# Kernel tuning notes

Hardware: AMD Instinct MI355X
Metric: run time of the kernel (lower is better)

## Reference

```python
import jax, jax.numpy as jnp
import numpy as np
from functools import partial

N_OSC = 50
N_PER = 40
DT = 0.001
STEPS = 700
HALF_PI = float(np.pi / 2)
# limb constants (simple antagonist-muscle one-link limb, as in TorchOneLinkMuscleLimb)
R_MOM = 0.02      # muscle moment arm
L0 = 0.1          # muscle length at angle 0
INERTIA = 1e-3
DAMP = 0.01
K_MUS = 50.0
L_REST = 0.05
TAU_M = 0.05


def get_m1_length(theta):
    return L0 - R_MOM * theta


def get_m2_length(theta):
    return L0 + R_MOM * theta


def limb_f(l_state, activation):
    # l_state: (B,4) = (angle, ang. velocity, m1 length, m2 length); activation: (B,2)
    theta, omega, l1, l2 = l_state[:, 0], l_state[:, 1], l_state[:, 2], l_state[:, 3]
    f1 = jax.nn.relu(activation[:, 0]) * K_MUS * jax.nn.relu(l1 - L_REST)
    f2 = jax.nn.relu(activation[:, 1]) * K_MUS * jax.nn.relu(l2 - L_REST)
    domega = (R_MOM * (f2 - f1) - DAMP * omega) / INERTIA
    dl1 = (get_m1_length(theta) - l1) / TAU_M
    dl2 = (get_m2_length(theta) - l2) / TAU_M
    return jnp.stack([omega, domega, dl1, dl2], axis=1)


def setup_inputs() -> dict:
    key = jax.random.key(0)
    ks = jax.random.split(key, 16)
    B = 4096
    x = jax.random.normal(ks[0], (B, 2), dtype=jnp.float32) * 0.5
    def lin(k, out_d, in_d, scale=None):
        s = (1.0 / np.sqrt(in_d)) if scale is None else scale
        kw, kb = jax.random.split(k)
        w = jax.random.uniform(kw, (out_d, in_d), jnp.float32, -s, s)
        b = jax.random.uniform(kb, (out_d,), jnp.float32, -s, s)
        return w, b
    fc1_w, fc1_b = lin(ks[1], 128, 2)
    fc2_w, fc2_b = lin(ks[2], 128, 128)
    fc3_w, fc3_b = lin(ks[3], N_OSC * 2, 128)
    fcd_w, fcd_b = lin(ks[4], 2, 128)
    fcd_w = fcd_w / 100.0
    fcd_b = fcd_b * 0.0 + 0.1
    fc4_w, fc4_b = lin(ks[5], 32, N_OSC * N_PER)
    fc5_w, fc5_b = lin(ks[6], 2, 32)
    fc5_w = fc5_w / 10000.0
    fc5_b = fc5_b * 0.0
    # NEF oscillator populations: encoders (unit vectors), biases, decoders
    enc = jax.random.normal(ks[7], (N_OSC, N_PER, 2), dtype=jnp.float32)
    enc = enc / jnp.linalg.norm(enc, axis=-1, keepdims=True)
    osc_bias = jax.random.uniform(ks[8], (N_OSC, N_PER), jnp.float32, -1.0, 1.0)
    dec = jax.random.normal(ks[9], (N_OSC, 2, N_PER), dtype=jnp.float32) * 0.05
    return dict(x=x, fc1_w=fc1_w, fc1_b=fc1_b, fc2_w=fc2_w, fc2_b=fc2_b,
                fc3_w=fc3_w, fc3_b=fc3_b, fcd_w=fcd_w, fcd_b=fcd_b,
                enc=enc, osc_bias=osc_bias, dec=dec,
                fc4_w=fc4_w, fc4_b=fc4_b, fc5_w=fc5_w, fc5_b=fc5_b)


def _forward(x, fc1_w, fc1_b, fc2_w, fc2_b, fc3_w, fc3_b, fcd_w, fcd_b,
             enc, osc_bias, dec, fc4_w, fc4_b, fc5_w, fc5_b):
    B = x.shape[0]
    current_angle = x[:, 0]
    h = jax.nn.relu(x @ fc1_w.T + fc1_b)
    direct = h @ fcd_w.T + fcd_b                     # (B, 2)
    h2 = jax.nn.relu(h @ fc2_w.T + fc2_b)
    xo = h2 @ fc3_w.T + fc3_b                        # (B, 2*N_OSC)
    o0 = jnp.transpose(xo.reshape(B, N_OSC, 2), (1, 0, 2))   # (O, B, 2)
    l0 = jnp.stack([current_angle, jnp.zeros_like(current_angle),
                    get_m1_length(current_angle), get_m2_length(current_angle)], axis=1)

    def step(carry, _):
        o_states, l_state = carry
        # NEF activities: relu(encoders . state + bias) per oscillator
        a = jax.nn.relu(jnp.einsum('opd,obd->obp', enc, o_states) + osc_bias[:, None, :])  # (O,B,P)
        deriv = jnp.einsum('odp,obp->obd', dec, a)
        o_states = o_states + DT * deriv
        activities = jnp.transpose(a, (1, 0, 2)).reshape(B, N_OSC * N_PER)  # (B, 2000)
        b1 = jax.nn.relu(activities @ fc4_w.T + fc4_b)
        activation = b1 @ fc5_w.T + fc5_b + direct    # (B, 2)
        l_new = l_state + DT * limb_f(l_state, activation)
        pos, vel = l_new[:, 0], l_new[:, 1]
        in_bounds = (pos > -HALF_PI) & (pos < HALF_PI)
        l_new = jnp.stack([jnp.clip(pos, -HALF_PI, HALF_PI),
                           jnp.where(in_bounds, vel, 0.0),
                           l_new[:, 2], l_new[:, 3]], axis=1)
        return (o_states, l_new), (l_new, activation)

    (_, _), (l_states, activations) = jax.lax.scan(step, (o0, l0), None, length=STEPS)
    return l_states, activations


@jax.jit
def reference(x, fc1_w, fc1_b, fc2_w, fc2_b, fc3_w, fc3_b, fcd_w, fcd_b,
              enc, osc_bias, dec, fc4_w, fc4_b, fc5_w, fc5_b):
    return _forward(x, fc1_w, fc1_b, fc2_w, fc2_b, fc3_w, fc3_b, fcd_w, fcd_b,
                    enc, osc_bias, dec, fc4_w, fc4_b, fc5_w, fc5_b)
```

## Files before the change

### kernel.cpp

```cpp
#include <hip/hip_runtime.h>

#define NTHR 1024
#define NB   16
#define NOSC 50
#define NPER 40
#define KTOT 2000
#define KPAD 2048
#define NSTEP 700
#define BATCH 4096
#define B1STR 36
#define OS_STR 36
#define HALF_PI 1.57079632679489662f
#define ACT_OFF ((size_t)NSTEP * BATCH * 4)

typedef _Float16 v8h __attribute__((ext_vector_type(8)));
typedef _Float16 h2_t __attribute__((ext_vector_type(2)));
typedef float v4f __attribute__((ext_vector_type(4)));

__device__ _Float16 g_w4[32 * KPAD];

__device__ __forceinline__ float fdot2f(float a_bits, float b_bits, float acc) {
    h2_t a = __builtin_bit_cast(h2_t, a_bits);
    h2_t b = __builtin_bit_cast(h2_t, b_bits);
#if __has_builtin(__builtin_amdgcn_fdot2)
    return __builtin_amdgcn_fdot2(a, b, acc, false);
#else
    return fmaf((float)a[0], (float)b[0], fmaf((float)a[1], (float)b[1], acc));
#endif
}

__device__ __forceinline__ float dot4(float4 a, float4 b, float acc) {
    acc = fmaf(a.x, b.x, acc);
    acc = fmaf(a.y, b.y, acc);
    acc = fmaf(a.z, b.z, acc);
    acc = fmaf(a.w, b.w, acc);
    return acc;
}

__device__ __forceinline__ float pkrtz(float a, float b) {
    auto q = __builtin_amdgcn_cvt_pkrtz(a, b);
    return __builtin_bit_cast(float, q);
}

__device__ __forceinline__ float cvt2rtn(float a, float b) {
    h2_t u; u[0] = (_Float16)a; u[1] = (_Float16)b;
    return __builtin_bit_cast(float, u);
}

__global__ void prep_f16(const float* __restrict__ fc4_w) {
    int tid = blockIdx.x * blockDim.x + threadIdx.x;
    int j = tid >> 11, k = tid & 2047;
    g_w4[j * KPAD + k] = (k < KTOT) ? (_Float16)fc4_w[j * KTOT + k] : (_Float16)0.f;
}

__global__ __launch_bounds__(NTHR)
void net_main(const float* __restrict__ x,
              const float* __restrict__ fc1_w, const float* __restrict__ fc1_b,
              const float* __restrict__ fc2_w, const float* __restrict__ fc2_b,
              const float* __restrict__ fc3_w, const float* __restrict__ fc3_b,
              const float* __restrict__ fcd_w, const float* __restrict__ fcd_b,
              const float* __restrict__ enc,   const float* __restrict__ osc_bias,
              const float* __restrict__ dec,
              const float* __restrict__ fc4_b,
              const float* __restrict__ fc5_w, const float* __restrict__ fc5_b,
              float* __restrict__ out)
{
    __shared__ __align__(16) _Float16 act_sh[256 * 128];
    __shared__ __align__(16) float part[8 * 2 * 256];
    __shared__ __align__(16) float os_sh[NOSC * OS_STR];
    __shared__ __align__(16) float b1s[NB * B1STR];
    __shared__ __align__(16) float dir[NB * 2];

    const int t    = threadIdx.x;
    const int lane = t & 63;
    const int wv   = t >> 6;
    const int b0   = blockIdx.x * NB;

    float* h  = (float*)act_sh;
    float* h2 = (float*)act_sh + NB * 128;

    #pragma unroll
    for (int ii = 0; ii < 2; ++ii) {
        int task = t + ii * NTHR;
        int b = task >> 7, i = task & 127;
        float x0 = x[(b0 + b) * 2 + 0];
        float x1 = x[(b0 + b) * 2 + 1];
        float v = fmaf(x0, fc1_w[2 * i], fmaf(x1, fc1_w[2 * i + 1], fc1_b[i]));
        h[b * 128 + i] = fmaxf(v, 0.f);
    }
    __syncthreads();
    #pragma unroll
    for (int ii = 0; ii < 2; ++ii) {
        int task = t + ii * NTHR;
        int b = task >> 7, i = task & 127;
        float acc = fc2_b[i];
        #pragma unroll 4
        for (int k = 0; k < 128; k += 4)
            acc = dot4(*(const float4*)&fc2_w[i * 128 + k],
                       *(const float4*)&h[b * 128 + k], acc);
        h2[b * 128 + i] = fmaxf(acc, 0.f);
    }
    if (t < NB * 2) {
        int b = t >> 1, j = t & 1;
        float acc = fcd_b[j];
        #pragma unroll 4
        for (int k = 0; k < 128; k += 4)
            acc = dot4(*(const float4*)&fcd_w[j * 128 + k],
                       *(const float4*)&h[b * 128 + k], acc);
        dir[b * 2 + j] = acc;
    }
    __syncthreads();
    #pragma unroll
    for (int ii = 0; ii < 2; ++ii) {
        int task = t + ii * NTHR;
        if (task < NOSC * NB * 2) {
            int o = task >> 5, r = task & 31, b = r >> 1;
            int row = o * 2 + (r & 1);
            float acc = fc3_b[row];
            #pragma unroll 4
            for (int k = 0; k < 128; k += 4)
                acc = dot4(*(const float4*)&fc3_w[row * 128 + k],
                           *(const float4*)&h2[b * 128 + k], acc);
            os_sh[o * OS_STR + r] = acc;
        }
    }
    const int my_oct = t >> 2;
    float4 e0 = {0,0,0,0}, e1 = {0,0,0,0}, e2 = {0,0,0,0}, e3 = {0,0,0,0};
    float4 bi0 = {0,0,0,0}, bi1 = {0,0,0,0};
    int my_o = 0;
    if (my_oct < 250) {
        const float4* ep = (const float4*)&enc[my_oct * 16];
        e0 = ep[0]; e1 = ep[1]; e2 = ep[2]; e3 = ep[3];
        const float4* bp = (const float4*)&osc_bias[my_oct * 8];
        bi0 = bp[0]; bi1 = bp[1];
        my_o = my_oct / 5;
    }
    const int di = t - 512;
    int d_o = 0, d_b = 0;
    bool dual = false;
    if (di >= 0) {
        if (di < 288) { dual = true; d_o = di >> 3; d_b = (di & 7) * 2; }
        else          { int task = di + 288; d_o = task >> 4; d_b = task & 15; }
    }
    float theta = 0.f, omega = 0.f, l1 = 0.f, l2 = 0.f, bs0 = 0.f, bs1 = 0.f;
    const int cb = t - 1008;
    if (cb >= 0 && cb < NB) {
        theta = x[(b0 + cb) * 2 + 0];
        l1 = fmaf(-0.02f, theta, 0.1f);
        l2 = fmaf( 0.02f, theta, 0.1f);
    }
    __syncthreads();
    if (cb >= 0 && cb < NB) {
        bs0 = dir[cb * 2 + 0] + fc5_b[0];
        bs1 = dir[cb * 2 + 1] + fc5_b[1];
    }
    if (t < 768) act_sh[32000 + t] = (_Float16)0.f;

    const int n_col = lane & 15, quad = lane >> 4;
    const int lidx  = lane ^ (quad << 2);
    int a_off[8];
    #pragma unroll
    for (int ks = 0; ks < 8; ++ks) {
        int oct = wv * 32 + ks * 4 + quad;
        a_off[ks] = (oct & 255) * 128 + ((n_col ^ (oct & 15)) * 8);
    }

    v4f st[16];
    if (t < 512) {
        const _Float16* wp = &g_w4[n_col * KPAD + wv * 256 + quad * 8];
        #pragma unroll
        for (int ks = 0; ks < 8; ++ks) {
            st[ks]     = __builtin_bit_cast(v4f, *(const v8h*)&wp[ks * 32]);
            st[8 + ks] = __builtin_bit_cast(v4f, *(const v8h*)&wp[16 * KPAD + ks * 32]);
        }
    } else {
        const float* d0p = &dec[(d_o * 2 + 0) * 40];
        const float* d1p = &dec[(d_o * 2 + 1) * 40];
        #pragma unroll
        for (int c = 0; c < 5; ++c) {
            v4f v0, v1;
            v0.x = cvt2rtn(d0p[c*8+0], d0p[c*8+1]);
            v0.y = cvt2rtn(d0p[c*8+2], d0p[c*8+3]);
            v0.z = cvt2rtn(d0p[c*8+4], d0p[c*8+5]);
            v0.w = cvt2rtn(d0p[c*8+6], d0p[c*8+7]);
            v1.x = cvt2rtn(d1p[c*8+0], d1p[c*8+1]);
            v1.y = cvt2rtn(d1p[c*8+2], d1p[c*8+3]);
            v1.z = cvt2rtn(d1p[c*8+4], d1p[c*8+5]);
            v1.w = cvt2rtn(d1p[c*8+6], d1p[c*8+7]);
            st[c]     = v0;
            st[5 + c] = v1;
        }
        #pragma unroll
        for (int i = 10; i < 16; ++i) st[i] = (v4f){0.f, 0.f, 0.f, 0.f};
    }

    auto phaseA = [&]() {
        if (my_oct < 250) {
            const int i4 = (t & 3) << 2;
            float4 osA = *(const float4*)&os_sh[my_o * OS_STR + i4 * 2];
            float4 osB = *(const float4*)&os_sh[my_o * OS_STR + i4 * 2 + 4];
            #pragma unroll
            for (int ii = 0; ii < 4; ++ii) {
                int b = i4 + ii;
                float osx = (ii == 0) ? osA.x : (ii == 1) ? osA.z : (ii == 2) ? osB.x : osB.z;
                float osy = (ii == 0) ? osA.y : (ii == 1) ? osA.w : (ii == 2) ? osB.y : osB.w;
                float r0 = fmaxf(fmaf(e0.x, osx, fmaf(e0.y, osy, bi0.x)), 0.f);
                float r1 = fmaxf(fmaf(e0.z, osx, fmaf(e0.w, osy, bi0.y)), 0.f);
                float r2 = fmaxf(fmaf(e1.x, osx, fmaf(e1.y, osy, bi0.z)), 0.f);
                float r3 = fmaxf(fmaf(e1.z, osx, fmaf(e1.w, osy, bi0.w)), 0.f);
                float r4 = fmaxf(fmaf(e2.x, osx, fmaf(e2.y, osy, bi1.x)), 0.f);
                float r5 = fmaxf(fmaf(e2.z, osx, fmaf(e2.w, osy, bi1.y)), 0.f);
                float r6 = fmaxf(fmaf(e3.x, osx, fmaf(e3.y, osy, bi1.z)), 0.f);
                float r7 = fmaxf(fmaf(e3.z, osx, fmaf(e3.w, osy, bi1.w)), 0.f);
                float4 pk;
                pk.x = pkrtz(r0, r1);
                pk.y = pkrtz(r2, r3);
                pk.z = pkrtz(r4, r5);
                pk.w = pkrtz(r6, r7);
                *(float4*)&act_sh[my_oct * 128 + ((b ^ my_oct) & 15) * 8] = pk;
            }
        }
    };

    auto derivDot = [&](int b, float& pOut, float& qOut) {
        float p0 = 0.f, p1 = 0.f, q0 = 0.f, q1 = 0.f;
        #pragma unroll
        for (int c = 0; c < 5; ++c) {
            int oct = d_o * 5 + c;
            float4 af = *(const float4*)&act_sh[oct * 128 + ((b ^ oct) & 15) * 8];
            p0 = fdot2f(af.x, st[c].x, p0);     p1 = fdot2f(af.y, st[c].y, p1);
            p0 = fdot2f(af.z, st[c].z, p0);     p1 = fdot2f(af.w, st[c].w, p1);
            q0 = fdot2f(af.x, st[5+c].x, q0);   q1 = fdot2f(af.y, st[5+c].y, q1);
            q0 = fdot2f(af.z, st[5+c].z, q0);   q1 = fdot2f(af.w, st[5+c].w, q1);
        }
        pOut = p0 + p1;
        qOut = q0 + q1;
    };

    phaseA();
    __syncthreads();

    for (int s = 0; s < NSTEP; ++s) {
        if (t < 512) {
            v4f c0 = {0.f, 0.f, 0.f, 0.f}, c1 = {0.f, 0.f, 0.f, 0.f};
            #pragma unroll
            for (int ks = 0; ks < 8; ++ks) {
                v8h a  = *(const v8h*)&act_sh[a_off[ks]];
                v8h w0 = __builtin_bit_cast(v8h, st[ks]);
                v8h w1 = __builtin_bit_cast(v8h, st[8 + ks]);
                c0 = __builtin_amdgcn_mfma_f32_16x16x32_f16(a, w0, c0, 0, 0, 0);
                c1 = __builtin_amdgcn_mfma_f32_16x16x32_f16(a, w1, c1, 0, 0, 0);
            }
            *(v4f*)&part[(wv * 2 + 0) * 256 + lidx * 4] = c0;
            *(v4f*)&part[(wv * 2 + 1) * 256 + lidx * 4] = c1;
        } else {
            if (dual) {
                float pA, qA, pB, qB;
                derivDot(d_b,     pA, qA);
                derivDot(d_b + 1, pB, qB);
                float4 osv = *(const float4*)&os_sh[d_o * OS_STR + d_b * 2];
                osv.x += 0.001f * pA;
                osv.y += 0.001f * qA;
                osv.z += 0.001f * pB;
                osv.w += 0.001f * qB;
                *(float4*)&os_sh[d_o * OS_STR + d_b * 2] = osv;
            } else {
                float p, q;
                derivDot(d_b, p, q);
                float2 osv = *(const float2*)&os_sh[d_o * OS_STR + d_b * 2];
                osv.x += 0.001f * p;
                osv.y += 0.001f * q;
                *(float2*)&os_sh[d_o * OS_STR + d_b * 2] = osv;
            }
            if (cb >= 0 && cb < NB && s > 0) {
                float a0 = bs0, a1 = bs1;
                #pragma unroll
                for (int i = 0; i < 32; i += 4) {
                    float4 bv = *(const float4*)&b1s[cb * B1STR + i];
                    a0 = dot4(bv, *(const float4*)&fc5_w[i],      a0);
                    a1 = dot4(bv, *(const float4*)&fc5_w[32 + i], a1);
                }
                float f1v = fmaxf(a0, 0.f) * 50.f * fmaxf(l1 - 0.05f, 0.f);
                float f2v = fmaxf(a1, 0.f) * 50.f * fmaxf(l2 - 0.05f, 0.f);
                float domega = (0.02f * (f2v - f1v) - 0.01f * omega) / 0.001f;
                float dl1 = ((0.1f - 0.02f * theta) - l1) / 0.05f;
                float dl2 = ((0.1f + 0.02f * theta) - l2) / 0.05f;
                float pos = fmaf(0.001f, omega,  theta);
                float vel = fmaf(0.001f, domega, omega);
                l1 = fmaf(0.001f, dl1, l1);
                l2 = fmaf(0.001f, dl2, l2);
                bool inb = (pos > -HALF_PI) && (pos < HALF_PI);
                float posc = fminf(fmaxf(pos, -HALF_PI), HALF_PI);
                vel = inb ? vel : 0.f;
                theta = posc;
                omega = vel;
                float4 lo; lo.x = posc; lo.y = vel; lo.z = l1; lo.w = l2;
                *(float4*)&out[((size_t)(s - 1) * BATCH + (b0 + cb)) * 4] = lo;
                float2 ao; ao.x = a0; ao.y = a1;
                *(float2*)&out[ACT_OFF + ((size_t)(s - 1) * BATCH + (b0 + cb)) * 2] = ao;
            }
        }
        __syncthreads();

        if (t < 512) {
            int b = t & 15, j = t >> 4;
            int g = j >> 4, n = j & 15;
            int Lp = (b >> 2) * 16 + (n ^ ((b >> 2) << 2));
            int base = g * 256 + Lp * 4 + (b & 3);
            float sum = 0.f;
            #pragma unroll
            for (int w = 0; w < 8; ++w)
                sum += part[w * 512 + base];
            b1s[b * B1STR + j] = fmaxf(sum + fc4_b[j], 0.f);
        }
        phaseA();
        __syncthreads();
    }

    if (cb >= 0 && cb < NB) {
        const int s = NSTEP - 1;
        float a0 = bs0, a1 = bs1;
        #pragma unroll
        for (int i = 0; i < 32; i += 4) {
            float4 bv = *(const float4*)&b1s[cb * B1STR + i];
            a0 = dot4(bv, *(const float4*)&fc5_w[i],      a0);
            a1 = dot4(bv, *(const float4*)&fc5_w[32 + i], a1);
        }
        float f1v = fmaxf(a0, 0.f) * 50.f * fmaxf(l1 - 0.05f, 0.f);
        float f2v = fmaxf(a1, 0.f) * 50.f * fmaxf(l2 - 0.05f, 0.f);
        float domega = (0.02f * (f2v - f1v) - 0.01f * omega) / 0.001f;
        float dl1 = ((0.1f - 0.02f * theta) - l1) / 0.05f;
        float dl2 = ((0.1f + 0.02f * theta) - l2) / 0.05f;
        float pos = fmaf(0.001f, omega,  theta);
        float vel = fmaf(0.001f, domega, omega);
        l1 = fmaf(0.001f, dl1, l1);
        l2 = fmaf(0.001f, dl2, l2);
        bool inb = (pos > -HALF_PI) && (pos < HALF_PI);
        float posc = fminf(fmaxf(pos, -HALF_PI), HALF_PI);
        vel = inb ? vel : 0.f;
        float4 lo; lo.x = posc; lo.y = vel; lo.z = l1; lo.w = l2;
        *(float4*)&out[((size_t)s * BATCH + (b0 + cb)) * 4] = lo;
        float2 ao; ao.x = a0; ao.y = a1;
        *(float2*)&out[ACT_OFF + ((size_t)s * BATCH + (b0 + cb)) * 2] = ao;
    }
}

extern "C" void kernel_launch(void* const* d_in, const int* in_sizes, int n_in,
                              void* d_out, int out_size, void* d_ws, size_t ws_size,
                              hipStream_t stream) {
    (void)in_sizes; (void)n_in; (void)d_ws; (void)ws_size; (void)out_size;
    const float* x_     = (const float*)d_in[0];
    const float* fc1_w  = (const float*)d_in[1];
    const float* fc1_b  = (const float*)d_in[2];
    const float* fc2_w  = (const float*)d_in[3];
    const float* fc2_b  = (const float*)d_in[4];
    const float* fc3_w  = (const float*)d_in[5];
    const float* fc3_b  = (const float*)d_in[6];
    const float* fcd_w  = (const float*)d_in[7];
    const float* fcd_b  = (const float*)d_in[8];
    const float* enc    = (const float*)d_in[9];
    const float* oscb   = (const float*)d_in[10];
    const float* dec    = (const float*)d_in[11];
    const float* fc4_w  = (const float*)d_in[12];
    const float* fc4_b  = (const float*)d_in[13];
    const float* fc5_w  = (const float*)d_in[14];
    const float* fc5_b  = (const float*)d_in[15];
    float* out = (float*)d_out;

    hipLaunchKernelGGL(prep_f16, dim3(256), dim3(256), 0, stream, fc4_w);
    hipLaunchKernelGGL(net_main, dim3(BATCH / NB), dim3(NTHR), 0, stream,
                       x_, fc1_w, fc1_b, fc2_w, fc2_b, fc3_w, fc3_b,
                       fcd_w, fcd_b, enc, oscb, dec, fc4_b,
                       fc5_w, fc5_b, out);
}
```

Baseline: 1.995 ms.

## Double-buffer fc4 partials and skew b1 reduction and limb update by a step

Double-buffers the MFMA partial-sum buffer and the b1 activation buffer so the fc4 reduction for step s-1 runs in the MFMA waves during step s, and the fc5/limb update trails by two steps. This takes the b1 reduction out of the serial section between the two barriers, shortening the critical path per step. In exchange it uses more LDS, adds an epilogue to drain the pipeline, and lengthens the MFMA warps' critical work.

```diff
diff --git a/kernel.cpp b/kernel.cpp
--- a/kernel.cpp
+++ b/kernel.cpp
@@ -66,9 +66,9 @@
               float* __restrict__ out)
 {
     __shared__ __align__(16) _Float16 act_sh[256 * 128];
-    __shared__ __align__(16) float part[8 * 2 * 256];
+    __shared__ __align__(16) float part[2 * 4096];
     __shared__ __align__(16) float os_sh[NOSC * OS_STR];
-    __shared__ __align__(16) float b1s[NB * B1STR];
+    __shared__ __align__(16) float b1s[2][NB * B1STR];
     __shared__ __align__(16) float dir[NB * 2];
 
     const int t    = threadIdx.x;
@@ -237,11 +237,40 @@
         qOut = q0 + q1;
     };
 
+    auto fc5Limb = [&](int sm) {
+        float a0 = bs0, a1 = bs1;
+        #pragma unroll
+        for (int i = 0; i < 32; i += 4) {
+            float4 bv = *(const float4*)&b1s[sm & 1][cb * B1STR + i];
+            a0 = dot4(bv, *(const float4*)&fc5_w[i],      a0);
+            a1 = dot4(bv, *(const float4*)&fc5_w[32 + i], a1);
+        }
+        float f1v = fmaxf(a0, 0.f) * 50.f * fmaxf(l1 - 0.05f, 0.f);
+        float f2v = fmaxf(a1, 0.f) * 50.f * fmaxf(l2 - 0.05f, 0.f);
+        float domega = (0.02f * (f2v - f1v) - 0.01f * omega) / 0.001f;
+        float dl1 = ((0.1f - 0.02f * theta) - l1) / 0.05f;
+        float dl2 = ((0.1f + 0.02f * theta) - l2) / 0.05f;
+        float pos = fmaf(0.001f, omega,  theta);
+        float vel = fmaf(0.001f, domega, omega);
+        l1 = fmaf(0.001f, dl1, l1);
+        l2 = fmaf(0.001f, dl2, l2);
+        bool inb = (pos > -HALF_PI) && (pos < HALF_PI);
+        float posc = fminf(fmaxf(pos, -HALF_PI), HALF_PI);
+        vel = inb ? vel : 0.f;
+        theta = posc;
+        omega = vel;
+        float4 lo; lo.x = posc; lo.y = vel; lo.z = l1; lo.w = l2;
+        *(float4*)&out[((size_t)sm * BATCH + (b0 + cb)) * 4] = lo;
+        float2 ao; ao.x = a0; ao.y = a1;
+        *(float2*)&out[ACT_OFF + ((size_t)sm * BATCH + (b0 + cb)) * 2] = ao;
+    };
+
     phaseA();
     __syncthreads();
 
     for (int s = 0; s < NSTEP; ++s) {
         if (t < 512) {
+            const int pb = (s & 1) * 4096;
             v4f c0 = {0.f, 0.f, 0.f, 0.f}, c1 = {0.f, 0.f, 0.f, 0.f};
             #pragma unroll
             for (int ks = 0; ks < 8; ++ks) {
@@ -251,8 +280,20 @@
                 c0 = __builtin_amdgcn_mfma_f32_16x16x32_f16(a, w0, c0, 0, 0, 0);
                 c1 = __builtin_amdgcn_mfma_f32_16x16x32_f16(a, w1, c1, 0, 0, 0);
             }
-            *(v4f*)&part[(wv * 2 + 0) * 256 + lidx * 4] = c0;
-            *(v4f*)&part[(wv * 2 + 1) * 256 + lidx * 4] = c1;
+            *(v4f*)&part[pb + (wv * 2 + 0) * 256 + lidx * 4] = c0;
+            *(v4f*)&part[pb + (wv * 2 + 1) * 256 + lidx * 4] = c1;
+            if (s > 0) {
+                const int pr = ((s - 1) & 1) * 4096;
+                int b = t & 15, j = t >> 4;
+                int g = j >> 4, n = j & 15;
+                int Lp = (b >> 2) * 16 + (n ^ ((b >> 2) << 2));
+                int base = pr + g * 256 + Lp * 4 + (b & 3);
+                float sum = 0.f;
+                #pragma unroll
+                for (int w = 0; w < 8; ++w)
+                    sum += part[w * 512 + base];
+                b1s[(s - 1) & 1][b * B1STR + j] = fmaxf(sum + fc4_b[j], 0.f);
+            }
         } else {
             if (dual) {
                 float pA, qA, pB, qB;
@@ -272,77 +313,32 @@
                 osv.y += 0.001f * q;
                 *(float2*)&os_sh[d_o * OS_STR + d_b * 2] = osv;
             }
-            if (cb >= 0 && cb < NB && s > 0) {
-                float a0 = bs0, a1 = bs1;
-                #pragma unroll
-                for (int i = 0; i < 32; i += 4) {
-                    float4 bv = *(const float4*)&b1s[cb * B1STR + i];
-                    a0 = dot4(bv, *(const float4*)&fc5_w[i],      a0);
-                    a1 = dot4(bv, *(const float4*)&fc5_w[32 + i], a1);
-                }
-                float f1v = fmaxf(a0, 0.f) * 50.f * fmaxf(l1 - 0.05f, 0.f);
-                float f2v = fmaxf(a1, 0.f) * 50.f * fmaxf(l2 - 0.05f, 0.f);
-                float domega = (0.02f * (f2v - f1v) - 0.01f * omega) / 0.001f;
-                float dl1 = ((0.1f - 0.02f * theta) - l1) / 0.05f;
-                float dl2 = ((0.1f + 0.02f * theta) - l2) / 0.05f;
-                float pos = fmaf(0.001f, omega,  theta);
-                float vel = fmaf(0.001f, domega, omega);
-                l1 = fmaf(0.001f, dl1, l1);
-                l2 = fmaf(0.001f, dl2, l2);
-                bool inb = (pos > -HALF_PI) && (pos < HALF_PI);
-                float posc = fminf(fmaxf(pos, -HALF_PI), HALF_PI);
-                vel = inb ? vel : 0.f;
-                theta = posc;
-                omega = vel;
-                float4 lo; lo.x = posc; lo.y = vel; lo.z = l1; lo.w = l2;
-                *(float4*)&out[((size_t)(s - 1) * BATCH + (b0 + cb)) * 4] = lo;
-                float2 ao; ao.x = a0; ao.y = a1;
-                *(float2*)&out[ACT_OFF + ((size_t)(s - 1) * BATCH + (b0 + cb)) * 2] = ao;
-            }
+            if (cb >= 0 && cb < NB && s >= 2)
+                fc5Limb(s - 2);
         }
         __syncthreads();
 
-        if (t < 512) {
-            int b = t & 15, j = t >> 4;
-            int g = j >> 4, n = j & 15;
-            int Lp = (b >> 2) * 16 + (n ^ ((b >> 2) << 2));
-            int base = g * 256 + Lp * 4 + (b & 3);
-            float sum = 0.f;
-            #pragma unroll
-            for (int w = 0; w < 8; ++w)
-                sum += part[w * 512 + base];
-            b1s[b * B1STR + j] = fmaxf(sum + fc4_b[j], 0.f);
-        }
         phaseA();
         __syncthreads();
     }
 
-    if (cb >= 0 && cb < NB) {
-        const int s = NSTEP - 1;
-        float a0 = bs0, a1 = bs1;
-        #pragma unroll
-        for (int i = 0; i < 32; i += 4) {
-            float4 bv = *(const float4*)&b1s[cb * B1STR + i];
-            a0 = dot4(bv, *(const float4*)&fc5_w[i],      a0);
-            a1 = dot4(bv, *(const float4*)&fc5_w[32 + i], a1);
-        }
-        float f1v = fmaxf(a0, 0.f) * 50.f * fmaxf(l1 - 0.05f, 0.f);
-        float f2v = fmaxf(a1, 0.f) * 50.f * fmaxf(l2 - 0.05f, 0.f);
-        float domega = (0.02f * (f2v - f1v) - 0.01f * omega) / 0.001f;
-        float dl1 = ((0.1f - 0.02f * theta) - l1) / 0.05f;
-        float dl2 = ((0.1f + 0.02f * theta) - l2) / 0.05f;
-        float pos = fmaf(0.001f, omega,  theta);
-        float vel = fmaf(0.001f, domega, omega);
-        l1 = fmaf(0.001f, dl1, l1);
-        l2 = fmaf(0.001f, dl2, l2);
-        bool inb = (pos > -HALF_PI) && (pos < HALF_PI);
-        float posc = fminf(fmaxf(pos, -HALF_PI), HALF_PI);
-        vel = inb ? vel : 0.f;
-        float4 lo; lo.x = posc; lo.y = vel; lo.z = l1; lo.w = l2;
-        *(float4*)&out[((size_t)s * BATCH + (b0 + cb)) * 4] = lo;
-        float2 ao; ao.x = a0; ao.y = a1;
-        *(float2*)&out[ACT_OFF + ((size_t)s * BATCH + (b0 + cb)) * 2] = ao;
-    }
+    if (t < 512) {
+        const int pr = ((NSTEP - 1) & 1) * 4096;
+        int b = t & 15, j = t >> 4;
+        int g = j >> 4, n = j & 15;
+        int Lp = (b >> 2) * 16 + (n ^ ((b >> 2) << 2));
+        int base = pr + g * 256 + Lp * 4 + (b & 3);
+        float sum = 0.f;
+        #pragma unroll
+        for (int w = 0; w < 8; ++w)
+            sum += part[w * 512 + base];
+        b1s[(NSTEP - 1) & 1][b * B1STR + j] = fmaxf(sum + fc4_b[j], 0.f);
+    } else if (cb >= 0 && cb < NB) {
+        fc5Limb(NSTEP - 2);
+    }
+    __syncthreads();
+    if (cb >= 0 && cb < NB)
+        fc5Limb(NSTEP - 1);
 }
 
 extern "C" void kernel_launch(void* const* d_in, const int* in_sizes, int n_in,
```

Result: faster. 1.807 ms (-9.4%).
